# Kernel tuning notes

Hardware: AMD Instinct MI355X
Metric: run time of the kernel (lower is better)

The kernel has to match this reference:

```python
import jax, jax.numpy as jnp
import numpy as np

ANCHOR_LENGTHS = jnp.array([1., 2., 3., 4., 5., 7., 9.], dtype=jnp.float32)  # A = 7


def make_anchors_1d(Lf):
    # anchors [Lf*A, 2] in feature coords, matching torch make_anchors_1d
    centers = jnp.arange(Lf, dtype=jnp.float32) + 0.5          # [Lf]
    c = centers[:, None]                                        # [Lf,1]
    w = ANCHOR_LENGTHS[None, :]                                 # [1,A]
    start = c - 0.5 * w
    end = c + 0.5 * w
    return jnp.stack(jnp.broadcast_arrays(start, end), axis=-1).reshape(-1, 2)


def setup_inputs() -> dict:
    key = jax.random.key(0)
    ks = jax.random.split(key, 4)
    B, C, Lf, A = 8, 512, 16384, 7
    feat = jax.random.normal(ks[0], (B, C, Lf), dtype=jnp.float32)
    conv_w = jax.random.normal(ks[1], (C, C, 3), dtype=jnp.float32) * 0.02
    conv_b = jnp.zeros((C,), dtype=jnp.float32)
    obj_w = jax.random.normal(ks[2], (A, C, 1), dtype=jnp.float32) * 0.02
    obj_b = jnp.zeros((A,), dtype=jnp.float32)
    reg_w = jax.random.normal(ks[3], (A * 2, C, 1), dtype=jnp.float32) * 0.02
    reg_b = jnp.zeros((A * 2,), dtype=jnp.float32)
    return {"feat": feat, "conv_w": conv_w, "conv_b": conv_b,
            "obj_w": obj_w, "obj_b": obj_b, "reg_w": reg_w, "reg_b": reg_b}


def reference(feat, conv_w, conv_b, obj_w, obj_b, reg_w, reg_b):
    B, C, Lf = feat.shape
    A = obj_w.shape[0]
    # conv1d k=3 pad=1 (NCH layout), + bias, relu
    h = jax.lax.conv_general_dilated(
        feat, conv_w, window_strides=(1,), padding=((1, 1),),
        dimension_numbers=("NCH", "OIH", "NCH"))
    h = jax.nn.relu(h + conv_b[None, :, None])                  # [B,C,Lf]
    # 1x1 heads as channel contractions
    obj = jnp.einsum("bcl,ac->bla", h, obj_w[:, :, 0]) + obj_b  # [B,Lf,A]
    reg = jnp.einsum("bcl,oc->blo", h, reg_w[:, :, 0]) + reg_b  # [B,Lf,2A]
    obj = obj.reshape(B, Lf * A)                                # [B,N]
    reg = reg.reshape(B, Lf, A, 2).reshape(B, Lf * A, 2)        # [B,N,2]
    anchors = make_anchors_1d(Lf)                               # [N,2]
    return obj, reg, anchors
```

## Files before the change

### kernel.cpp

```cpp
#include <hip/hip_runtime.h>
#include <hip/hip_bf16.h>
#include <stdint.h>

typedef __attribute__((ext_vector_type(4))) float f32x4;
typedef __attribute__((ext_vector_type(16))) float f32x16;
typedef __attribute__((ext_vector_type(4))) int i32x4;
typedef __attribute__((ext_vector_type(8))) int i32x8;
typedef __attribute__((ext_vector_type(8))) short bh8;
typedef unsigned short u16;
typedef unsigned int u32;
typedef unsigned char u8;

#define B_    8
#define C_    512
#define LF    16384
#define KTOT  1536
#define SCL   0x7F7F7F7Fu

#define P4_BYTES ((size_t)4 * B_ * 21 * LF * 4)
#define W8_OFF   P4_BYTES

#define OBJ_OFF  0
#define REG_OFF  917504
#define ANC_OFF  2752512

__device__ __forceinline__ u32 pk2bf(float lo, float hi) {
    u32 r;
    asm("v_cvt_pk_bf16_f32 %0, %1, %2" : "=v"(r) : "v"(lo), "v"(hi));
    return r;
}
__device__ __forceinline__ void gload16(const u8* g, u8* l) {
    __builtin_amdgcn_global_load_lds(
        (const __attribute__((address_space(1))) void*)g,
        (__attribute__((address_space(3))) void*)l, 16, 0, 0);
}

__global__ void k_cast_w(const float* __restrict__ cw, u8* __restrict__ W8) {
    int i = blockIdx.x * 256 + threadIdx.x;
    if (i >= C_ * KTOT / 2) return;
    int co = i / (KTOT / 2);
    int rr = (i % (KTOT / 2)) * 2;
    int t = rr / 512, q = rr % 512;
    int kc = q >> 6, cc = q & 63;
    int jl = (cc >> 4) ^ ((co >> 1) & 3);
    int ci = kc * 64 + jl * 16 + (cc & 15);
    float f0 = cw[(co * C_ + ci) * 3 + t];
    float f1 = cw[(co * C_ + ci + 1) * 3 + t];
    u32 pk = __builtin_amdgcn_cvt_pk_fp8_f32(f0, f1, 0, false);
    *(u16*)&W8[(size_t)co * KTOT + rr] = (u16)pk;
}

__global__ void k_anchors(float* __restrict__ out) {
    int l = blockIdx.x * 256 + threadIdx.x;
    if (l >= LF) return;
    const float AL[7] = {1.f, 2.f, 3.f, 4.f, 5.f, 7.f, 9.f};
    float c = (float)l + 0.5f;
    float* an = out + ANC_OFF + (size_t)l * 14;
#pragma unroll
    for (int a = 0; a < 7; ++a) {
        an[a * 2 + 0] = c - 0.5f * AL[a];
        an[a * 2 + 1] = c + 0.5f * AL[a];
    }
}

__global__ __launch_bounds__(256, 3) void k_conv_head(
    const float* __restrict__ feat, const u8* __restrict__ W8,
    const float* __restrict__ conv_b, const float* __restrict__ obj_w,
    const float* __restrict__ reg_w, float* __restrict__ P4) {
    __shared__ __align__(16) char smem[40960];
    u8* As3 = (u8*)smem;
    u8* Bs  = (u8*)(smem + 24576);
    u16* Hs = (u16*)smem;
    u16* Wp = (u16*)(smem + 32768);

    const int tid = threadIdx.x;
    const int lane = tid & 63, wave = tid >> 6;
    const int wm = wave >> 1, wn = wave & 1;
    const int g = lane >> 4, cL = lane & 15;
    const int r32 = lane & 31, hK = lane >> 5;

    const int wg = (blockIdx.x & 7) * 512 + (blockIdx.x >> 3);
    const int mt = wg & 3;
    const int l0 = ((wg >> 2) & 127) * 128;
    const int b  = wg >> 9;
    const int co0 = mt * 128;

    const int cg = tid & 15, lgrp = tid >> 4;

    f32x16 acc[2][2];
#pragma unroll
    for (int mi = 0; mi < 2; ++mi)
#pragma unroll
        for (int ni = 0; ni < 2; ++ni)
#pragma unroll
            for (int r = 0; r < 16; ++r) acc[mi][ni][r] = 0.f;

    for (int kc = 0; kc < 8; ++kc) {
        __syncthreads();
#pragma unroll
        for (int t = 0; t < 3; ++t)
#pragma unroll
            for (int p = 0; p < 2; ++p) {
                const int row = p * 64 + (tid >> 2);
                const int colB = (tid & 3) * 16;
                gload16(&W8[(size_t)(co0 + row) * KTOT + t * 512 + kc * 64 + colB],
                        &As3[t * 8192 + row * 64 + colB]);
            }
        {
            const float* fp = feat +
                ((size_t)(b * C_ + kc * 64 + cg * 4)) * LF + l0 + lgrp * 8;
            const int slog = cg >> 2;
            const int soff = (cg * 4) & 15;
#pragma unroll
            for (int h = 0; h < 2; ++h) {
                float4 v0 = *(const float4*)(fp + 0 * LF + h * 4);
                float4 v1 = *(const float4*)(fp + 1 * LF + h * 4);
                float4 v2 = *(const float4*)(fp + 2 * LF + h * 4);
                float4 v3 = *(const float4*)(fp + 3 * LF + h * 4);
#pragma unroll
                for (int e = 0; e < 4; ++e) {
                    const int r = 1 + lgrp * 8 + h * 4 + e;
                    u32 w0 = __builtin_amdgcn_cvt_pk_fp8_f32(
                        ((const float*)&v0)[e], ((const float*)&v1)[e], 0, false);
                    u32 w  = __builtin_amdgcn_cvt_pk_fp8_f32(
                        ((const float*)&v2)[e], ((const float*)&v3)[e], w0, true);
                    const int pc = ((slog ^ ((r >> 1) & 3)) * 16) + soff;
                    *(u32*)&Bs[r * 64 + pc] = w;
                }
            }
        }
        if (tid < 128) {
            const int ci2 = tid >> 1;
            const int rr = (tid & 1) ? 129 : 0;
            const int l = l0 + ((tid & 1) ? 128 : -1);
            float v = (l >= 0 && l < LF)
                          ? feat[((size_t)(b * C_ + kc * 64 + ci2)) * LF + l]
                          : 0.f;
            u32 p = __builtin_amdgcn_cvt_pk_fp8_f32(v, 0.f, 0, false);
            const int pc = (((ci2 >> 4) ^ ((rr >> 1) & 3)) * 16) + (ci2 & 15);
            Bs[rr * 64 + pc] = (u8)p;
        }
        __syncthreads();
#pragma unroll
        for (int t = 0; t < 3; ++t) {
            const u8* At = As3 + t * 8192;
            i32x8 af[2], bf[2];
#pragma unroll
            for (int mi = 0; mi < 2; ++mi) {
                const int row = wm * 64 + mi * 32 + r32;
                const int x = (row >> 1) & 3;
                i32x4 a0 = *(const i32x4*)&At[row * 64 + (((2 * hK) ^ x) * 16)];
                i32x4 a1 = *(const i32x4*)&At[row * 64 + (((2 * hK + 1) ^ x) * 16)];
                af[mi] = __builtin_shufflevector(a0, a1, 0, 1, 2, 3, 4, 5, 6, 7);
            }
#pragma unroll
            for (int ni = 0; ni < 2; ++ni) {
                const int row = wn * 64 + ni * 32 + r32 + t;
                const int x = (row >> 1) & 3;
                i32x4 b0 = *(const i32x4*)&Bs[row * 64 + (((2 * hK) ^ x) * 16)];
                i32x4 b1 = *(const i32x4*)&Bs[row * 64 + (((2 * hK + 1) ^ x) * 16)];
                bf[ni] = __builtin_shufflevector(b0, b1, 0, 1, 2, 3, 4, 5, 6, 7);
            }
#pragma unroll
            for (int mi = 0; mi < 2; ++mi)
#pragma unroll
                for (int ni = 0; ni < 2; ++ni)
                    acc[mi][ni] = __builtin_amdgcn_mfma_scale_f32_32x32x64_f8f6f4(
                        af[mi], bf[ni], acc[mi][ni], 0, 0, 0, SCL, 0, SCL);
        }
    }
    __syncthreads();

#pragma unroll
    for (int mi = 0; mi < 2; ++mi)
#pragma unroll
        for (int ni = 0; ni < 2; ++ni) {
            const int l_loc = wn * 64 + ni * 32 + r32;
            const int xw = (l_loc & 7) << 3;
#pragma unroll
            for (int q = 0; q < 4; ++q) {
                const int cb = wm * 64 + mi * 32 + q * 8 + 4 * hK;
                const float b0_ = conv_b[co0 + cb + 0];
                const float b1_ = conv_b[co0 + cb + 1];
                const float b2_ = conv_b[co0 + cb + 2];
                const float b3_ = conv_b[co0 + cb + 3];
                uint2 pk;
                pk.x = pk2bf(fmaxf(acc[mi][ni][q * 4 + 0] + b0_, 0.f),
                             fmaxf(acc[mi][ni][q * 4 + 1] + b1_, 0.f));
                pk.y = pk2bf(fmaxf(acc[mi][ni][q * 4 + 2] + b2_, 0.f),
                             fmaxf(acc[mi][ni][q * 4 + 3] + b3_, 0.f));
                *(uint2*)&Hs[l_loc * 128 + (cb ^ xw)] = pk;
            }
        }
#pragma unroll
    for (int it = 0; it < 4; ++it) {
        const int q = it * 256 + tid;
        const int a = q >> 5, c0 = (q & 31) * 4;
        float4 wv = {0.f, 0.f, 0.f, 0.f};
        if (a < 7)       wv = *(const float4*)&obj_w[a * C_ + co0 + c0];
        else if (a < 21) wv = *(const float4*)&reg_w[(a - 7) * C_ + co0 + c0];
        uint2 pk;
        pk.x = pk2bf(wv.x, wv.y);
        pk.y = pk2bf(wv.z, wv.w);
        *(uint2*)&Wp[a * 128 + (c0 ^ ((a & 7) << 3))] = pk;
    }
    __syncthreads();

    f32x4 hacc[2][2];
#pragma unroll
    for (int m = 0; m < 2; ++m)
#pragma unroll
        for (int n = 0; n < 2; ++n) hacc[m][n] = {0.f, 0.f, 0.f, 0.f};
    const int ln0 = wave * 32;
    const int swA = (cL & 7) << 3;
#pragma unroll
    for (int ks2 = 0; ks2 < 4; ++ks2) {
        const int ko = ks2 * 32 + g * 8;
        bh8 wa[2], hb[2];
        wa[0] = *(const bh8*)&Wp[cL * 128 + (ko ^ swA)];
        wa[1] = *(const bh8*)&Wp[(16 + cL) * 128 + (ko ^ swA)];
        hb[0] = *(const bh8*)&Hs[(ln0 + cL) * 128 + (ko ^ swA)];
        hb[1] = *(const bh8*)&Hs[(ln0 + 16 + cL) * 128 + (ko ^ swA)];
#pragma unroll
        for (int m = 0; m < 2; ++m)
#pragma unroll
            for (int n = 0; n < 2; ++n)
                hacc[m][n] = __builtin_amdgcn_mfma_f32_16x16x32_bf16(
                    wa[m], hb[n], hacc[m][n], 0, 0, 0);
    }
    float* P4base = P4 + ((size_t)(mt * B_ + b) * 21) * LF + l0;
#pragma unroll
    for (int m = 0; m < 2; ++m) {
        const int a0 = m * 16 + g * 4;
#pragma unroll
        for (int n = 0; n < 2; ++n) {
            const int l = ln0 + n * 16 + cL;
#pragma unroll
            for (int r = 0; r < 4; ++r) {
                const int a = a0 + r;
                if (a < 21) P4base[(size_t)a * LF + l] = hacc[m][n][r];
            }
        }
    }
}

__global__ void k_finalize(const float* __restrict__ P4, const float* __restrict__ obj_b,
                           const float* __restrict__ reg_b, float* __restrict__ out) {
    int gid = blockIdx.x * 256 + threadIdx.x;
    if (gid >= B_ * LF) return;
    int b = gid >> 14, l = gid & (LF - 1);
    float s[21];
#pragma unroll
    for (int a = 0; a < 21; ++a) {
        float v = 0.f;
#pragma unroll
        for (int m = 0; m < 4; ++m) v += P4[((size_t)(m * B_ + b) * 21 + a) * LF + l];
        s[a] = v;
    }
    float* op = out + OBJ_OFF + (size_t)b * (LF * 7) + (size_t)l * 7;
#pragma unroll
    for (int a = 0; a < 7; ++a) op[a] = s[a] + obj_b[a];
    float* rp = out + REG_OFF + (size_t)b * (LF * 14) + (size_t)l * 14;
#pragma unroll
    for (int o = 0; o < 14; ++o) rp[o] = s[7 + o] + reg_b[o];
}

extern "C" void kernel_launch(void* const* d_in, const int* in_sizes, int n_in,
                              void* d_out, int out_size, void* d_ws, size_t ws_size,
                              hipStream_t stream) {
    const float* feat   = (const float*)d_in[0];
    const float* conv_w = (const float*)d_in[1];
    const float* conv_b = (const float*)d_in[2];
    const float* obj_w  = (const float*)d_in[3];
    const float* obj_b  = (const float*)d_in[4];
    const float* reg_w  = (const float*)d_in[5];
    const float* reg_b  = (const float*)d_in[6];
    char* ws = (char*)d_ws;
    float* P4 = (float*)ws;
    u8* W8    = (u8*)(ws + W8_OFF);
    float* out = (float*)d_out;

    k_cast_w<<<1536, 256, 0, stream>>>(conv_w, W8);
    k_anchors<<<64, 256, 0, stream>>>(out);
    k_conv_head<<<4096, 256, 0, stream>>>(feat, W8, conv_b, obj_w, reg_w, P4);
    k_finalize<<<(B_ * LF + 255) / 256, 256, 0, stream>>>(P4, obj_b, reg_b, out);
}
```

Measured before the change: 229.0 us.

## Halve conv tile along length to 64 for higher occupancy

The L tile per workgroup shrinks from 128 to 64 positions, which doubles the grid to 8192 blocks. Accumulator registers and shared memory per block drop (smem 40KB to ~28KB), and launch bounds rise from 3 to 5 blocks per CU. The aim is more latency hiding from extra resident waves. In exchange, each A (weight) tile is reused over half as many columns, so weight traffic and halo overhead per output roughly double, and MFMA work per LDS load falls.

Result: slower. 269.3 us (+17.6%).

```diff
diff --git a/kernel.cpp b/kernel.cpp
--- a/kernel.cpp
+++ b/kernel.cpp
@@ -63,15 +63,15 @@
     }
 }
 
-__global__ __launch_bounds__(256, 3) void k_conv_head(
+__global__ __launch_bounds__(256, 5) void k_conv_head(
     const float* __restrict__ feat, const u8* __restrict__ W8,
     const float* __restrict__ conv_b, const float* __restrict__ obj_w,
     const float* __restrict__ reg_w, float* __restrict__ P4) {
-    __shared__ __align__(16) char smem[40960];
+    __shared__ __align__(16) char smem[28800];
     u8* As3 = (u8*)smem;
     u8* Bs  = (u8*)(smem + 24576);
     u16* Hs = (u16*)smem;
-    u16* Wp = (u16*)(smem + 32768);
+    u16* Wp = (u16*)(smem + 16384);
 
     const int tid = threadIdx.x;
     const int lane = tid & 63, wave = tid >> 6;
@@ -79,21 +79,19 @@
     const int g = lane >> 4, cL = lane & 15;
     const int r32 = lane & 31, hK = lane >> 5;
 
-    const int wg = (blockIdx.x & 7) * 512 + (blockIdx.x >> 3);
+    const int wg = (blockIdx.x & 7) * 1024 + (blockIdx.x >> 3);
     const int mt = wg & 3;
-    const int l0 = ((wg >> 2) & 127) * 128;
-    const int b  = wg >> 9;
+    const int l0 = ((wg >> 2) & 255) * 64;
+    const int b  = wg >> 10;
     const int co0 = mt * 128;
 
     const int cg = tid & 15, lgrp = tid >> 4;
 
-    f32x16 acc[2][2];
+    f32x16 acc[2];
 #pragma unroll
     for (int mi = 0; mi < 2; ++mi)
 #pragma unroll
-        for (int ni = 0; ni < 2; ++ni)
-#pragma unroll
-            for (int r = 0; r < 16; ++r) acc[mi][ni][r] = 0.f;
+        for (int r = 0; r < 16; ++r) acc[mi][r] = 0.f;
 
     for (int kc = 0; kc < 8; ++kc) {
         __syncthreads();
@@ -108,31 +106,28 @@
             }
         {
             const float* fp = feat +
-                ((size_t)(b * C_ + kc * 64 + cg * 4)) * LF + l0 + lgrp * 8;
+                ((size_t)(b * C_ + kc * 64 + cg * 4)) * LF + l0 + lgrp * 4;
+            float4 v0 = *(const float4*)(fp + 0 * LF);
+            float4 v1 = *(const float4*)(fp + 1 * LF);
+            float4 v2 = *(const float4*)(fp + 2 * LF);
+            float4 v3 = *(const float4*)(fp + 3 * LF);
             const int slog = cg >> 2;
             const int soff = (cg * 4) & 15;
 #pragma unroll
-            for (int h = 0; h < 2; ++h) {
-                float4 v0 = *(const float4*)(fp + 0 * LF + h * 4);
-                float4 v1 = *(const float4*)(fp + 1 * LF + h * 4);
-                float4 v2 = *(const float4*)(fp + 2 * LF + h * 4);
-                float4 v3 = *(const float4*)(fp + 3 * LF + h * 4);
-#pragma unroll
-                for (int e = 0; e < 4; ++e) {
-                    const int r = 1 + lgrp * 8 + h * 4 + e;
-                    u32 w0 = __builtin_amdgcn_cvt_pk_fp8_f32(
-                        ((const float*)&v0)[e], ((const float*)&v1)[e], 0, false);
-                    u32 w  = __builtin_amdgcn_cvt_pk_fp8_f32(
-                        ((const float*)&v2)[e], ((const float*)&v3)[e], w0, true);
-                    const int pc = ((slog ^ ((r >> 1) & 3)) * 16) + soff;
-                    *(u32*)&Bs[r * 64 + pc] = w;
-                }
+            for (int e = 0; e < 4; ++e) {
+                const int r = 1 + lgrp * 4 + e;
+                u32 w0 = __builtin_amdgcn_cvt_pk_fp8_f32(
+                    ((const float*)&v0)[e], ((const float*)&v1)[e], 0, false);
+                u32 w  = __builtin_amdgcn_cvt_pk_fp8_f32(
+                    ((const float*)&v2)[e], ((const float*)&v3)[e], w0, true);
+                const int pc = ((slog ^ ((r >> 1) & 3)) * 16) + soff;
+                *(u32*)&Bs[r * 64 + pc] = w;
             }
         }
         if (tid < 128) {
             const int ci2 = tid >> 1;
-            const int rr = (tid & 1) ? 129 : 0;
-            const int l = l0 + ((tid & 1) ? 128 : -1);
+            const int rr = (tid & 1) ? 65 : 0;
+            const int l = l0 + ((tid & 1) ? 64 : -1);
             float v = (l >= 0 && l < LF)
                           ? feat[((size_t)(b * C_ + kc * 64 + ci2)) * LF + l]
                           : 0.f;
@@ -144,7 +139,7 @@
 #pragma unroll
         for (int t = 0; t < 3; ++t) {
             const u8* At = As3 + t * 8192;
-            i32x8 af[2], bf[2];
+            i32x8 af[2], bf;
 #pragma unroll
             for (int mi = 0; mi < 2; ++mi) {
                 const int row = wm * 64 + mi * 32 + r32;
@@ -153,45 +148,40 @@
                 i32x4 a1 = *(const i32x4*)&At[row * 64 + (((2 * hK + 1) ^ x) * 16)];
                 af[mi] = __builtin_shufflevector(a0, a1, 0, 1, 2, 3, 4, 5, 6, 7);
             }
-#pragma unroll
-            for (int ni = 0; ni < 2; ++ni) {
-                const int row = wn * 64 + ni * 32 + r32 + t;
+            {
+                const int row = wn * 32 + r32 + t;
                 const int x = (row >> 1) & 3;
                 i32x4 b0 = *(const i32x4*)&Bs[row * 64 + (((2 * hK) ^ x) * 16)];
                 i32x4 b1 = *(const i32x4*)&Bs[row * 64 + (((2 * hK + 1) ^ x) * 16)];
-                bf[ni] = __builtin_shufflevector(b0, b1, 0, 1, 2, 3, 4, 5, 6, 7);
+                bf = __builtin_shufflevector(b0, b1, 0, 1, 2, 3, 4, 5, 6, 7);
             }
 #pragma unroll
             for (int mi = 0; mi < 2; ++mi)
-#pragma unroll
-                for (int ni = 0; ni < 2; ++ni)
-                    acc[mi][ni] = __builtin_amdgcn_mfma_scale_f32_32x32x64_f8f6f4(
-                        af[mi], bf[ni], acc[mi][ni], 0, 0, 0, SCL, 0, SCL);
+                acc[mi] = __builtin_amdgcn_mfma_scale_f32_32x32x64_f8f6f4(
+                    af[mi], bf, acc[mi], 0, 0, 0, SCL, 0, SCL);
         }
     }
     __syncthreads();
 
 #pragma unroll
-    for (int mi = 0; mi < 2; ++mi)
-#pragma unroll
-        for (int ni = 0; ni < 2; ++ni) {
-            const int l_loc = wn * 64 + ni * 32 + r32;
-            const int xw = (l_loc & 7) << 3;
-#pragma unroll
-            for (int q = 0; q < 4; ++q) {
-                const int cb = wm * 64 + mi * 32 + q * 8 + 4 * hK;
-                const float b0_ = conv_b[co0 + cb + 0];
-                const float b1_ = conv_b[co0 + cb + 1];
-                const float b2_ = conv_b[co0 + cb + 2];
-                const float b3_ = conv_b[co0 + cb + 3];
-                uint2 pk;
-                pk.x = pk2bf(fmaxf(acc[mi][ni][q * 4 + 0] + b0_, 0.f),
-                             fmaxf(acc[mi][ni][q * 4 + 1] + b1_, 0.f));
-                pk.y = pk2bf(fmaxf(acc[mi][ni][q * 4 + 2] + b2_, 0.f),
-                             fmaxf(acc[mi][ni][q * 4 + 3] + b3_, 0.f));
-                *(uint2*)&Hs[l_loc * 128 + (cb ^ xw)] = pk;
-            }
-        }
+    for (int mi = 0; mi < 2; ++mi) {
+        const int l_loc = wn * 32 + r32;
+        const int xw = (l_loc & 7) << 3;
+#pragma unroll
+        for (int q = 0; q < 4; ++q) {
+            const int cb = wm * 64 + mi * 32 + q * 8 + 4 * hK;
+            const float b0_ = conv_b[co0 + cb + 0];
+            const float b1_ = conv_b[co0 + cb + 1];
+            const float b2_ = conv_b[co0 + cb + 2];
+            const float b3_ = conv_b[co0 + cb + 3];
+            uint2 pk;
+            pk.x = pk2bf(fmaxf(acc[mi][q * 4 + 0] + b0_, 0.f),
+                         fmaxf(acc[mi][q * 4 + 1] + b1_, 0.f));
+            pk.y = pk2bf(fmaxf(acc[mi][q * 4 + 2] + b2_, 0.f),
+                         fmaxf(acc[mi][q * 4 + 3] + b3_, 0.f));
+            *(uint2*)&Hs[l_loc * 128 + (cb ^ xw)] = pk;
+        }
+    }
 #pragma unroll
     for (int it = 0; it < 4; ++it) {
         const int q = it * 256 + tid;
@@ -206,40 +196,29 @@
     }
     __syncthreads();
 
-    f32x4 hacc[2][2];
-#pragma unroll
-    for (int m = 0; m < 2; ++m)
-#pragma unroll
-        for (int n = 0; n < 2; ++n) hacc[m][n] = {0.f, 0.f, 0.f, 0.f};
-    const int ln0 = wave * 32;
+    f32x4 hacc[2];
+    hacc[0] = {0.f, 0.f, 0.f, 0.f};
+    hacc[1] = {0.f, 0.f, 0.f, 0.f};
+    const int ln0 = wave * 16;
     const int swA = (cL & 7) << 3;
 #pragma unroll
     for (int ks2 = 0; ks2 < 4; ++ks2) {
         const int ko = ks2 * 32 + g * 8;
-        bh8 wa[2], hb[2];
-        wa[0] = *(const bh8*)&Wp[cL * 128 + (ko ^ swA)];
-        wa[1] = *(const bh8*)&Wp[(16 + cL) * 128 + (ko ^ swA)];
-        hb[0] = *(const bh8*)&Hs[(ln0 + cL) * 128 + (ko ^ swA)];
-        hb[1] = *(const bh8*)&Hs[(ln0 + 16 + cL) * 128 + (ko ^ swA)];
-#pragma unroll
-        for (int m = 0; m < 2; ++m)
-#pragma unroll
-            for (int n = 0; n < 2; ++n)
-                hacc[m][n] = __builtin_amdgcn_mfma_f32_16x16x32_bf16(
-                    wa[m], hb[n], hacc[m][n], 0, 0, 0);
+        bh8 wa0 = *(const bh8*)&Wp[cL * 128 + (ko ^ swA)];
+        bh8 wa1 = *(const bh8*)&Wp[(16 + cL) * 128 + (ko ^ swA)];
+        bh8 hb  = *(const bh8*)&Hs[(ln0 + cL) * 128 + (ko ^ swA)];
+        hacc[0] = __builtin_amdgcn_mfma_f32_16x16x32_bf16(wa0, hb, hacc[0], 0, 0, 0);
+        hacc[1] = __builtin_amdgcn_mfma_f32_16x16x32_bf16(wa1, hb, hacc[1], 0, 0, 0);
     }
     float* P4base = P4 + ((size_t)(mt * B_ + b) * 21) * LF + l0;
 #pragma unroll
     for (int m = 0; m < 2; ++m) {
         const int a0 = m * 16 + g * 4;
-#pragma unroll
-        for (int n = 0; n < 2; ++n) {
-            const int l = ln0 + n * 16 + cL;
-#pragma unroll
-            for (int r = 0; r < 4; ++r) {
-                const int a = a0 + r;
-                if (a < 21) P4base[(size_t)a * LF + l] = hacc[m][n][r];
-            }
+        const int l = ln0 + cL;
+#pragma unroll
+        for (int r = 0; r < 4; ++r) {
+            const int a = a0 + r;
+            if (a < 21) P4base[(size_t)a * LF + l] = hacc[m][r];
         }
     }
 }
@@ -282,6 +261,6 @@
 
     k_cast_w<<<1536, 256, 0, stream>>>(conv_w, W8);
     k_anchors<<<64, 256, 0, stream>>>(out);
-    k_conv_head<<<4096, 256, 0, stream>>>(feat, W8, conv_b, obj_w, reg_w, P4);
+    k_conv_head<<<8192, 256, 0, stream>>>(feat, W8, conv_b, obj_w, reg_w, P4);
     k_finalize<<<(B_ * LF + 255) / 256, 256, 0, stream>>>(P4, obj_b, reg_b, out);
 }
```

## Load conv weight fragments directly from global memory and double-buffer the feature tile

Applied to the files above, without the earlier changes.

Conv weight fragments for the MFMA are now read straight from global memory into registers rather than staged through LDS with global_load_lds. The weight layout drops its XOR swizzle and becomes plain contiguous, and the feature tile alternates between two LDS buffers per k-chunk, which lets the leading barrier go. The goal is lower LDS traffic and fewer synchronisations per k-chunk. The cost is that every wave re-reads weights from global/L2 and load latency sits directly in front of the MFMAs.

Result: slower. 339.1 us (+48.1%).

```diff
diff --git a/kernel.cpp b/kernel.cpp
--- a/kernel.cpp
+++ b/kernel.cpp
@@ -29,21 +29,13 @@
     asm("v_cvt_pk_bf16_f32 %0, %1, %2" : "=v"(r) : "v"(lo), "v"(hi));
     return r;
 }
-__device__ __forceinline__ void gload16(const u8* g, u8* l) {
-    __builtin_amdgcn_global_load_lds(
-        (const __attribute__((address_space(1))) void*)g,
-        (__attribute__((address_space(3))) void*)l, 16, 0, 0);
-}
 
 __global__ void k_cast_w(const float* __restrict__ cw, u8* __restrict__ W8) {
     int i = blockIdx.x * 256 + threadIdx.x;
     if (i >= C_ * KTOT / 2) return;
     int co = i / (KTOT / 2);
     int rr = (i % (KTOT / 2)) * 2;
-    int t = rr / 512, q = rr % 512;
-    int kc = q >> 6, cc = q & 63;
-    int jl = (cc >> 4) ^ ((co >> 1) & 3);
-    int ci = kc * 64 + jl * 16 + (cc & 15);
+    int t = rr / 512, ci = rr % 512;
     float f0 = cw[(co * C_ + ci) * 3 + t];
     float f1 = cw[(co * C_ + ci + 1) * 3 + t];
     u32 pk = __builtin_amdgcn_cvt_pk_fp8_f32(f0, f1, 0, false);
@@ -68,8 +60,6 @@
     const float* __restrict__ conv_b, const float* __restrict__ obj_w,
     const float* __restrict__ reg_w, float* __restrict__ P4) {
     __shared__ __align__(16) char smem[40960];
-    u8* As3 = (u8*)smem;
-    u8* Bs  = (u8*)(smem + 24576);
     u16* Hs = (u16*)smem;
     u16* Wp = (u16*)(smem + 32768);
 
@@ -87,6 +77,8 @@
 
     const int cg = tid & 15, lgrp = tid >> 4;
 
+    const u8* Abase = W8 + (size_t)(co0 + wm * 64 + r32) * KTOT + hK * 32;
+
     f32x16 acc[2][2];
 #pragma unroll
     for (int mi = 0; mi < 2; ++mi)
@@ -96,16 +88,7 @@
             for (int r = 0; r < 16; ++r) acc[mi][ni][r] = 0.f;
 
     for (int kc = 0; kc < 8; ++kc) {
-        __syncthreads();
-#pragma unroll
-        for (int t = 0; t < 3; ++t)
-#pragma unroll
-            for (int p = 0; p < 2; ++p) {
-                const int row = p * 64 + (tid >> 2);
-                const int colB = (tid & 3) * 16;
-                gload16(&W8[(size_t)(co0 + row) * KTOT + t * 512 + kc * 64 + colB],
-                        &As3[t * 8192 + row * 64 + colB]);
-            }
+        u8* Bs = (u8*)smem + (kc & 1) * 8448;
         {
             const float* fp = feat +
                 ((size_t)(b * C_ + kc * 64 + cg * 4)) * LF + l0 + lgrp * 8;
@@ -143,14 +126,12 @@
         __syncthreads();
 #pragma unroll
         for (int t = 0; t < 3; ++t) {
-            const u8* At = As3 + t * 8192;
             i32x8 af[2], bf[2];
 #pragma unroll
             for (int mi = 0; mi < 2; ++mi) {
-                const int row = wm * 64 + mi * 32 + r32;
-                const int x = (row >> 1) & 3;
-                i32x4 a0 = *(const i32x4*)&At[row * 64 + (((2 * hK) ^ x) * 16)];
-                i32x4 a1 = *(const i32x4*)&At[row * 64 + (((2 * hK + 1) ^ x) * 16)];
+                const u8* ap = Abase + (size_t)mi * 32 * KTOT + t * 512 + kc * 64;
+                i32x4 a0 = *(const i32x4*)ap;
+                i32x4 a1 = *(const i32x4*)(ap + 16);
                 af[mi] = __builtin_shufflevector(a0, a1, 0, 1, 2, 3, 4, 5, 6, 7);
             }
 #pragma unroll
```

## Split head epilogue into two halves to shrink LDS and raise occupancy

Applied to the files above, without the earlier changes.

The bf16 hidden tile used by the 1x1 head GEMM is now staged half at a time (64 positions per pass) instead of all 128. This lets the head weights move to a lower LDS offset and cuts shared memory from 40960 to 33024 bytes, so launch bounds can ask for 4 blocks per CU instead of 3. The cost is an extra pair of barriers, serialised half passes in the epilogue, and tighter register limits under the higher occupancy target.

After: 225.9 us. No clear change (-1.4%).

```diff
diff --git a/kernel.cpp b/kernel.cpp
--- a/kernel.cpp
+++ b/kernel.cpp
@@ -63,15 +63,15 @@
     }
 }
 
-__global__ __launch_bounds__(256, 3) void k_conv_head(
+__global__ __launch_bounds__(256, 4) void k_conv_head(
     const float* __restrict__ feat, const u8* __restrict__ W8,
     const float* __restrict__ conv_b, const float* __restrict__ obj_w,
     const float* __restrict__ reg_w, float* __restrict__ P4) {
-    __shared__ __align__(16) char smem[40960];
+    __shared__ __align__(16) char smem[33024];
     u8* As3 = (u8*)smem;
     u8* Bs  = (u8*)(smem + 24576);
     u16* Hs = (u16*)smem;
-    u16* Wp = (u16*)(smem + 32768);
+    u16* Wp = (u16*)(smem + 16384);
 
     const int tid = threadIdx.x;
     const int lane = tid & 63, wave = tid >> 6;
@@ -172,27 +172,6 @@
     __syncthreads();
 
 #pragma unroll
-    for (int mi = 0; mi < 2; ++mi)
-#pragma unroll
-        for (int ni = 0; ni < 2; ++ni) {
-            const int l_loc = wn * 64 + ni * 32 + r32;
-            const int xw = (l_loc & 7) << 3;
-#pragma unroll
-            for (int q = 0; q < 4; ++q) {
-                const int cb = wm * 64 + mi * 32 + q * 8 + 4 * hK;
-                const float b0_ = conv_b[co0 + cb + 0];
-                const float b1_ = conv_b[co0 + cb + 1];
-                const float b2_ = conv_b[co0 + cb + 2];
-                const float b3_ = conv_b[co0 + cb + 3];
-                uint2 pk;
-                pk.x = pk2bf(fmaxf(acc[mi][ni][q * 4 + 0] + b0_, 0.f),
-                             fmaxf(acc[mi][ni][q * 4 + 1] + b1_, 0.f));
-                pk.y = pk2bf(fmaxf(acc[mi][ni][q * 4 + 2] + b2_, 0.f),
-                             fmaxf(acc[mi][ni][q * 4 + 3] + b3_, 0.f));
-                *(uint2*)&Hs[l_loc * 128 + (cb ^ xw)] = pk;
-            }
-        }
-#pragma unroll
     for (int it = 0; it < 4; ++it) {
         const int q = it * 256 + tid;
         const int a = q >> 5, c0 = (q & 31) * 4;
@@ -204,43 +183,60 @@
         pk.y = pk2bf(wv.z, wv.w);
         *(uint2*)&Wp[a * 128 + (c0 ^ ((a & 7) << 3))] = pk;
     }
-    __syncthreads();
-
-    f32x4 hacc[2][2];
-#pragma unroll
-    for (int m = 0; m < 2; ++m)
-#pragma unroll
-        for (int n = 0; n < 2; ++n) hacc[m][n] = {0.f, 0.f, 0.f, 0.f};
-    const int ln0 = wave * 32;
-    const int swA = (cL & 7) << 3;
-#pragma unroll
-    for (int ks2 = 0; ks2 < 4; ++ks2) {
-        const int ko = ks2 * 32 + g * 8;
-        bh8 wa[2], hb[2];
-        wa[0] = *(const bh8*)&Wp[cL * 128 + (ko ^ swA)];
-        wa[1] = *(const bh8*)&Wp[(16 + cL) * 128 + (ko ^ swA)];
-        hb[0] = *(const bh8*)&Hs[(ln0 + cL) * 128 + (ko ^ swA)];
-        hb[1] = *(const bh8*)&Hs[(ln0 + 16 + cL) * 128 + (ko ^ swA)];
-#pragma unroll
-        for (int m = 0; m < 2; ++m)
-#pragma unroll
-            for (int n = 0; n < 2; ++n)
-                hacc[m][n] = __builtin_amdgcn_mfma_f32_16x16x32_bf16(
-                    wa[m], hb[n], hacc[m][n], 0, 0, 0);
-    }
+
     float* P4base = P4 + ((size_t)(mt * B_ + b) * 21) * LF + l0;
 #pragma unroll
-    for (int m = 0; m < 2; ++m) {
-        const int a0 = m * 16 + g * 4;
-#pragma unroll
-        for (int n = 0; n < 2; ++n) {
-            const int l = ln0 + n * 16 + cL;
+    for (int half = 0; half < 2; ++half) {
+        if (wn == half) {
+#pragma unroll
+            for (int mi = 0; mi < 2; ++mi)
+#pragma unroll
+                for (int ni = 0; ni < 2; ++ni) {
+                    const int l_half = ni * 32 + r32;
+                    const int xw = (l_half & 7) << 3;
+#pragma unroll
+                    for (int q = 0; q < 4; ++q) {
+                        const int cb = wm * 64 + mi * 32 + q * 8 + 4 * hK;
+                        const float b0_ = conv_b[co0 + cb + 0];
+                        const float b1_ = conv_b[co0 + cb + 1];
+                        const float b2_ = conv_b[co0 + cb + 2];
+                        const float b3_ = conv_b[co0 + cb + 3];
+                        uint2 pk;
+                        pk.x = pk2bf(fmaxf(acc[mi][ni][q * 4 + 0] + b0_, 0.f),
+                                     fmaxf(acc[mi][ni][q * 4 + 1] + b1_, 0.f));
+                        pk.y = pk2bf(fmaxf(acc[mi][ni][q * 4 + 2] + b2_, 0.f),
+                                     fmaxf(acc[mi][ni][q * 4 + 3] + b3_, 0.f));
+                        *(uint2*)&Hs[l_half * 128 + (cb ^ xw)] = pk;
+                    }
+                }
+        }
+        __syncthreads();
+
+        f32x4 hacc0 = {0.f, 0.f, 0.f, 0.f};
+        f32x4 hacc1 = {0.f, 0.f, 0.f, 0.f};
+        const int lrow = wave * 16 + cL;
+        const int swA = (cL & 7) << 3;
+#pragma unroll
+        for (int ks2 = 0; ks2 < 4; ++ks2) {
+            const int ko = ks2 * 32 + g * 8;
+            bh8 wa0 = *(const bh8*)&Wp[cL * 128 + (ko ^ swA)];
+            bh8 wa1 = *(const bh8*)&Wp[(16 + cL) * 128 + (ko ^ swA)];
+            bh8 hb  = *(const bh8*)&Hs[lrow * 128 + (ko ^ swA)];
+            hacc0 = __builtin_amdgcn_mfma_f32_16x16x32_bf16(wa0, hb, hacc0, 0, 0, 0);
+            hacc1 = __builtin_amdgcn_mfma_f32_16x16x32_bf16(wa1, hb, hacc1, 0, 0, 0);
+        }
+        const int lg = half * 64 + lrow;
+#pragma unroll
+        for (int m = 0; m < 2; ++m) {
+            const int a0 = m * 16 + g * 4;
+            const f32x4 hv = (m == 0) ? hacc0 : hacc1;
 #pragma unroll
             for (int r = 0; r < 4; ++r) {
                 const int a = a0 + r;
-                if (a < 21) P4base[(size_t)a * LF + l] = hacc[m][n][r];
-            }
-        }
+                if (a < 21) P4base[(size_t)a * LF + lg] = hv[r];
+            }
+        }
+        __syncthreads();
     }
 }
 
```
